# Kernel optimization log

Measured on AMD Instinct MI355X. Metric: run time of the kernel, lower is better.

Reference implementation:

```python
import math
import jax, jax.numpy as jnp
import numpy as np

B, C, H, W = 4, 64, 128, 128
A = 64           # attention_size
OUT = 64         # output_size
KS = 3           # kernel_size
M = (KS - 1) // 2
SCALE = A ** (-0.5)


def _lin(x, Wt, b):
    return x @ Wt + b


def _pos_encoding(d_model, seq_len):
    # sinusoidal PE over the k^2 neighborhood positions; d_model even here
    pos = jnp.arange(seq_len, dtype=jnp.float32)[:, None]
    div = jnp.exp(jnp.arange(0, d_model, 2, dtype=jnp.float32) * (-math.log(10000.0) / d_model))
    s = jnp.sin(pos * div)   # (seq, d/2)
    c = jnp.cos(pos * div)
    return jnp.stack([s, c], axis=-1).reshape(seq_len, d_model)  # interleaved sin/cos


def _expand_shift(k_nchw):
    # k_nchw: (b, c, h, w) -> (b, c, h, w, KS*KS) neighbor gather (zero padded)
    h, w = k_nchw.shape[2], k_nchw.shape[3]
    p = jnp.pad(k_nchw, ((0, 0), (0, 0), (M, M), (M, M)))
    slices = [p[:, :, i:i + h, j:j + w] for i in range(KS) for j in range(KS)]
    return jnp.stack(slices, axis=-1)


def setup_inputs() -> dict:
    key = jax.random.key(0)
    ks = jax.random.split(key, 12)
    sd = lambda fan_in: 1.0 / math.sqrt(fan_in)
    return {
        "x": jax.random.normal(ks[0], (B, C, H, W), jnp.float32),
        "ln_g": jnp.ones((C,), jnp.float32),
        "ln_b": jnp.zeros((C,), jnp.float32),
        "Wq": jax.random.normal(ks[1], (C, 2 * A), jnp.float32) * sd(C),
        "bq": jnp.zeros((2 * A,), jnp.float32),
        "Wq2": jax.random.normal(ks[2], (2 * A, A), jnp.float32) * sd(2 * A),
        "bq2": jnp.zeros((A,), jnp.float32),
        "Wk": jax.random.normal(ks[3], (C, 2 * A), jnp.float32) * sd(C),
        "bk": jnp.zeros((2 * A,), jnp.float32),
        "Wk2": jax.random.normal(ks[4], (2 * A, A), jnp.float32) * sd(2 * A),
        "bk2": jnp.zeros((A,), jnp.float32),
        "Wv": jax.random.normal(ks[5], (C, 2 * A), jnp.float32) * sd(C),
        "bv": jnp.zeros((2 * A,), jnp.float32),
        "Wv2": jax.random.normal(ks[6], (2 * A, OUT), jnp.float32) * sd(2 * A),
        "bv2": jnp.zeros((OUT,), jnp.float32),
        "Wpos": jax.random.normal(ks[7], (C, A), jnp.float32) * sd(C),
        "bpos": jnp.zeros((A,), jnp.float32),
        "Wposk": jax.random.normal(ks[8], (A, A), jnp.float32) * sd(A),
        "bposk": jnp.zeros((A,), jnp.float32),
    }


def reference(x, ln_g, ln_b, Wq, bq, Wq2, bq2, Wk, bk, Wk2, bk2,
              Wv, bv, Wv2, bv2, Wpos, bpos, Wposk, bposk):
    # positional embedding over the 9 neighborhood slots
    pe = _pos_encoding(C, KS * KS)                       # (9, C)
    pos_emb = jax.nn.relu(_lin(pe, Wpos, bpos))          # (9, A)

    xn = jnp.transpose(x, (0, 2, 3, 1))                  # (b, h, w, c)
    mu = jnp.mean(xn, axis=-1, keepdims=True)
    var = jnp.mean((xn - mu) ** 2, axis=-1, keepdims=True)
    xn = (xn - mu) * jax.lax.rsqrt(var + 1e-5) * ln_g + ln_b

    K = _lin(jax.nn.relu(_lin(xn, Wk, bk)), Wk2, bk2)    # (b, h, w, A)
    Ksh = _expand_shift(jnp.transpose(K, (0, 3, 1, 2)))  # (b, A, h, w, 9)
    pos_k = jnp.transpose(_lin(pos_emb, Wposk, bposk))   # (A, 9)
    Kfull = Ksh + pos_k[None, :, None, None, :]

    Q = _lin(jax.nn.relu(_lin(xn, Wq, bq)), Wq2, bq2)    # (b, h, w, A)
    V = _lin(jax.nn.relu(_lin(xn, Wv, bv)), Wv2, bv2)    # (b, h, w, OUT)
    Vsh = _expand_shift(jnp.transpose(V, (0, 3, 1, 2)))  # (b, OUT, h, w, 9)

    att = jnp.einsum('bhwa,bahwp->bphw', Q, Kfull) * SCALE
    att = jax.nn.softmax(att, axis=1)                    # softmax over 9 neighbors
    out = jnp.einsum('bchwn,bnhw->bchw', Vsh, att)       # (b, OUT, h, w)
    return out  # stride == 1 -> no subsampling
```

## Files before the change

### kernel.cpp

```cpp
#include <hip/hip_runtime.h>
#include <hip/hip_bf16.h>
#include <math.h>

typedef __attribute__((ext_vector_type(8))) short short8;
typedef __attribute__((ext_vector_type(4))) float float4v;
typedef unsigned short ushort_t;
typedef unsigned int uint_t;

#define HWPIX 16384
#define NPIX  65536

__device__ inline float b2f(ushort_t u) {
    uint_t x = ((uint_t)u) << 16;
    return __builtin_bit_cast(float, x);
}
__device__ inline ushort_t f2b(float f) {
    uint_t x = __builtin_bit_cast(uint_t, f);
    uint_t r = (x + 0x7fffu + ((x >> 16) & 1u)) >> 16;
    return (ushort_t)r;
}
__device__ inline bool probe_bf16(const void* lng) {
    return *(const uint_t*)lng == 0x3F803F80u;
}
__device__ inline float ldf(const void* p, int i, bool bf) {
    return bf ? b2f(((const ushort_t*)p)[i]) : ((const float*)p)[i];
}
__device__ inline void unpack8(uint4 u, float* f) {
    f[0] = b2f((ushort_t)(u.x & 0xffff)); f[1] = b2f((ushort_t)(u.x >> 16));
    f[2] = b2f((ushort_t)(u.y & 0xffff)); f[3] = b2f((ushort_t)(u.y >> 16));
    f[4] = b2f((ushort_t)(u.z & 0xffff)); f[5] = b2f((ushort_t)(u.z >> 16));
    f[6] = b2f((ushort_t)(u.w & 0xffff)); f[7] = b2f((ushort_t)(u.w >> 16));
}

__global__ __launch_bounds__(256) void prep_kernel(
        const void* __restrict__ Wq, const void* __restrict__ Wq2,
        const void* __restrict__ Wk, const void* __restrict__ Wk2,
        const void* __restrict__ Wv, const void* __restrict__ Wv2,
        const void* __restrict__ Wpos, const void* __restrict__ bpos,
        const void* __restrict__ Wposk, const void* __restrict__ bposk,
        const void* __restrict__ lng,
        ushort_t* __restrict__ W1f, ushort_t* __restrict__ W2f, float* __restrict__ pk) {
    bool bf = probe_bf16(lng);
    if (blockIdx.x < 96) {
        int idx = blockIdx.x * 256 + threadIdx.x;
        int chain = idx >> 13;
        int o = idx & 8191;
        const void* W1 = chain == 0 ? Wq : (chain == 1 ? Wk : Wv);
        const void* W2 = chain == 0 ? Wq2 : (chain == 1 ? Wk2 : Wv2);
        {
            int j = o & 7, L = (o >> 3) & 63, nt = (o >> 9) & 7, kc = o >> 12;
            int k = kc * 32 + ((L >> 4) << 3) + j, n = nt * 16 + (L & 15);
            W1f[chain * 8192 + o] = f2b(ldf(W1, k * 128 + n, bf));
        }
        {
            int j = o & 7, L = (o >> 3) & 63, nt = (o >> 9) & 3, kc = (o >> 11) & 3;
            int k = kc * 32 + ((L >> 4) << 3) + j, n = nt * 16 + (L & 15);
            W2f[chain * 8192 + o] = f2b(ldf(W2, k * 64 + n, bf));
        }
    } else {
        __shared__ float pe[9][64];
        __shared__ float pemb[9][64];
        int t = threadIdx.x;
        for (int it = t; it < 576; it += 256) {
            int p = it >> 6, a = it & 63;
            int i = a >> 1;
            float div = expf(-(float)(2 * i) * 0.14391156831212787f);
            float ang = (float)p * div;
            pe[p][a] = (a & 1) ? cosf(ang) : sinf(ang);
        }
        __syncthreads();
        for (int it = t; it < 576; it += 256) {
            int p = it >> 6, a = it & 63;
            float s = ldf(bpos, a, bf);
            for (int c = 0; c < 64; ++c) s += pe[p][c] * ldf(Wpos, c * 64 + a, bf);
            pemb[p][a] = fmaxf(s, 0.f);
        }
        __syncthreads();
        for (int it = t; it < 576; it += 256) {
            int p = it >> 6, a = it & 63;
            float s = ldf(bposk, a, bf);
            for (int j = 0; j < 64; ++j) s += pemb[p][j] * ldf(Wposk, j * 64 + a, bf);
            pk[a * 9 + p] = s;
        }
    }
}

__global__ __launch_bounds__(256) void lnqkv_kernel(
        const void* __restrict__ x, const void* __restrict__ g, const void* __restrict__ bb,
        const ushort_t* __restrict__ W1f, const ushort_t* __restrict__ W2f,
        const void* __restrict__ b1q, const void* __restrict__ b1k, const void* __restrict__ b1v,
        const void* __restrict__ b2q, const void* __restrict__ b2k, const void* __restrict__ b2v,
        const void* __restrict__ lng,
        ushort_t* __restrict__ Qo, ushort_t* __restrict__ Ko, ushort_t* __restrict__ Vo) {
    bool bf = probe_bf16(lng);
    int tid = threadIdx.x;
    int wave = tid >> 6, lane = tid & 63;
    int q = lane >> 4, r = lane & 15;
    int pix0 = blockIdx.x * 64 + wave * 16;
    int b = pix0 >> 14;
    int sp = (pix0 & 16383) + r;

    float xl[8], xh[8];
    if (bf) {
        const ushort_t* xb = (const ushort_t*)x + (size_t)b * 64 * HWPIX + sp;
#pragma unroll
        for (int j = 0; j < 8; ++j) {
            xl[j] = b2f(xb[(size_t)(q * 8 + j) * HWPIX]);
            xh[j] = b2f(xb[(size_t)(32 + q * 8 + j) * HWPIX]);
        }
    } else {
        const float* xb = (const float*)x + (size_t)b * 64 * HWPIX + sp;
#pragma unroll
        for (int j = 0; j < 8; ++j) {
            xl[j] = xb[(size_t)(q * 8 + j) * HWPIX];
            xh[j] = xb[(size_t)(32 + q * 8 + j) * HWPIX];
        }
    }
    float s1 = 0.f, s2 = 0.f;
#pragma unroll
    for (int j = 0; j < 8; ++j) {
        s1 += xl[j] + xh[j];
        s2 += xl[j] * xl[j] + xh[j] * xh[j];
    }
    s1 += __shfl_xor(s1, 16); s2 += __shfl_xor(s2, 16);
    s1 += __shfl_xor(s1, 32); s2 += __shfl_xor(s2, 32);
    float mu = s1 * (1.f / 64.f);
    float var = s2 * (1.f / 64.f) - mu * mu;
    float rstd = rsqrtf(var + 1e-5f);

    short8 a0, a1;
#pragma unroll
    for (int j = 0; j < 8; ++j) {
        int c = q * 8 + j;
        float v = (xl[j] - mu) * rstd * ldf(g, c, bf) + ldf(bb, c, bf);
        a0[j] = (short)f2b(v);
        c += 32;
        v = (xh[j] - mu) * rstd * ldf(g, c, bf) + ldf(bb, c, bf);
        a1[j] = (short)f2b(v);
    }

    __shared__ __align__(16) ushort_t hid[4][16][136];

#pragma unroll
    for (int chain = 0; chain < 3; ++chain) {
        const ushort_t* W1 = W1f + chain * 8192;
        const ushort_t* W2 = W2f + chain * 8192;
        const void* b1 = chain == 0 ? b1q : (chain == 1 ? b1k : b1v);
        const void* b2 = chain == 0 ? b2q : (chain == 1 ? b2k : b2v);
        ushort_t* out = chain == 0 ? Qo : (chain == 1 ? Ko : Vo);

#pragma unroll
        for (int nt = 0; nt < 8; ++nt) {
            short8 bf0 = *reinterpret_cast<const short8*>(W1 + ((0 * 8 + nt) * 64 + lane) * 8);
            short8 bf1 = *reinterpret_cast<const short8*>(W1 + ((1 * 8 + nt) * 64 + lane) * 8);
            float4v acc = {0.f, 0.f, 0.f, 0.f};
            acc = __builtin_amdgcn_mfma_f32_16x16x32_bf16(a0, bf0, acc, 0, 0, 0);
            acc = __builtin_amdgcn_mfma_f32_16x16x32_bf16(a1, bf1, acc, 0, 0, 0);
            int n = nt * 16 + r;
            float bias = ldf(b1, n, bf);
#pragma unroll
            for (int rr = 0; rr < 4; ++rr) {
                float v = fmaxf(acc[rr] + bias, 0.f);
                hid[wave][q * 4 + rr][n] = f2b(v);
            }
        }
        short8 ha[4];
#pragma unroll
        for (int kc = 0; kc < 4; ++kc)
            ha[kc] = *reinterpret_cast<const short8*>(&hid[wave][r][kc * 32 + q * 8]);

#pragma unroll
        for (int nt = 0; nt < 4; ++nt) {
            float4v acc = {0.f, 0.f, 0.f, 0.f};
#pragma unroll
            for (int kc = 0; kc < 4; ++kc) {
                short8 bfr = *reinterpret_cast<const short8*>(W2 + ((kc * 4 + nt) * 64 + lane) * 8);
                acc = __builtin_amdgcn_mfma_f32_16x16x32_bf16(ha[kc], bfr, acc, 0, 0, 0);
            }
            int n = nt * 16 + r;
            float bias = ldf(b2, n, bf);
#pragma unroll
            for (int rr = 0; rr < 4; ++rr) {
                out[(size_t)(pix0 + q * 4 + rr) * 64 + n] = f2b(acc[rr] + bias);
            }
        }
    }
}

__global__ __launch_bounds__(256) void attn_kernel(
        const ushort_t* __restrict__ Q, const ushort_t* __restrict__ K,
        const ushort_t* __restrict__ V, const float* __restrict__ pk,
        const void* __restrict__ lng, void* __restrict__ out) {
    bool bf = probe_bf16(lng);
    int p = blockIdx.x * 256 + threadIdx.x;
    int b = p >> 14;
    int sp = p & 16383;
    int h = sp >> 7, w = sp & 127;

    float v64[64];
    const ushort_t* qp = Q + (size_t)p * 64;
#pragma unroll
    for (int c0 = 0; c0 < 64; c0 += 8) {
        uint4 u = *reinterpret_cast<const uint4*>(qp + c0);
        unpack8(u, &v64[c0]);
    }

    float s[9];
#pragma unroll
    for (int n = 0; n < 9; ++n) {
        int dy = n / 3 - 1, dx = n % 3 - 1;
        int hh = h + dy, ww = w + dx;
        float dot = 0.f;
#pragma unroll
        for (int c = 0; c < 64; ++c) dot += v64[c] * pk[c * 9 + n];
        if (hh >= 0 && hh < 128 && ww >= 0 && ww < 128) {
            const ushort_t* kp = K + ((size_t)(b << 14) + (size_t)(hh * 128 + ww)) * 64;
#pragma unroll
            for (int c0 = 0; c0 < 64; c0 += 8) {
                uint4 u = *reinterpret_cast<const uint4*>(kp + c0);
                float kv[8];
                unpack8(u, kv);
#pragma unroll
                for (int j = 0; j < 8; ++j) dot += v64[c0 + j] * kv[j];
            }
        }
        s[n] = dot * 0.125f;
    }
    float m = s[0];
#pragma unroll
    for (int n = 1; n < 9; ++n) m = fmaxf(m, s[n]);
    float sum = 0.f;
#pragma unroll
    for (int n = 0; n < 9; ++n) { s[n] = expf(s[n] - m); sum += s[n]; }
    float inv = 1.f / sum;

#pragma unroll
    for (int c = 0; c < 64; ++c) v64[c] = 0.f;
#pragma unroll
    for (int n = 0; n < 9; ++n) {
        int dy = n / 3 - 1, dx = n % 3 - 1;
        int hh = h + dy, ww = w + dx;
        if (hh < 0 || hh >= 128 || ww < 0 || ww >= 128) continue;
        float a = s[n] * inv;
        const ushort_t* vp = V + ((size_t)(b << 14) + (size_t)(hh * 128 + ww)) * 64;
#pragma unroll
        for (int c0 = 0; c0 < 64; c0 += 8) {
            uint4 u = *reinterpret_cast<const uint4*>(vp + c0);
            float vv[8];
            unpack8(u, vv);
#pragma unroll
            for (int j = 0; j < 8; ++j) v64[c0 + j] += a * vv[j];
        }
    }
    if (bf) {
        ushort_t* ob = (ushort_t*)out + ((size_t)b * 64) * HWPIX + sp;
#pragma unroll
        for (int c = 0; c < 64; ++c) ob[(size_t)c * HWPIX] = f2b(v64[c]);
    } else {
        float* ob = (float*)out + ((size_t)b * 64) * HWPIX + sp;
#pragma unroll
        for (int c = 0; c < 64; ++c) ob[(size_t)c * HWPIX] = v64[c];
    }
}

extern "C" void kernel_launch(void* const* d_in, const int* in_sizes, int n_in,
                              void* d_out, int out_size, void* d_ws, size_t ws_size,
                              hipStream_t stream) {
    (void)in_sizes; (void)n_in; (void)out_size; (void)ws_size;
    const void* x     = d_in[0];
    const void* ln_g  = d_in[1];
    const void* ln_b  = d_in[2];
    const void* Wq    = d_in[3];
    const void* bq    = d_in[4];
    const void* Wq2   = d_in[5];
    const void* bq2   = d_in[6];
    const void* Wk    = d_in[7];
    const void* bk    = d_in[8];
    const void* Wk2   = d_in[9];
    const void* bk2   = d_in[10];
    const void* Wv    = d_in[11];
    const void* bv    = d_in[12];
    const void* Wv2   = d_in[13];
    const void* bv2   = d_in[14];
    const void* Wpos  = d_in[15];
    const void* bpos  = d_in[16];
    const void* Wposk = d_in[17];
    const void* bposk = d_in[18];

    char* ws = (char*)d_ws;
    ushort_t* Qo  = (ushort_t*)(ws);
    ushort_t* Ko  = (ushort_t*)(ws + (size_t)8 * 1024 * 1024);
    ushort_t* Vo  = (ushort_t*)(ws + (size_t)16 * 1024 * 1024);
    ushort_t* W1f = (ushort_t*)(ws + (size_t)24 * 1024 * 1024);
    ushort_t* W2f = (ushort_t*)(ws + (size_t)24 * 1024 * 1024 + 65536);
    float*    pk  = (float*)(ws + (size_t)24 * 1024 * 1024 + 131072);

    prep_kernel<<<97, 256, 0, stream>>>(Wq, Wq2, Wk, Wk2, Wv, Wv2,
                                        Wpos, bpos, Wposk, bposk, ln_g, W1f, W2f, pk);
    lnqkv_kernel<<<1024, 256, 0, stream>>>(x, ln_g, ln_b, W1f, W2f,
                                           bq, bk, bv, bq2, bk2, bv2, ln_g, Qo, Ko, Vo);
    attn_kernel<<<256, 256, 0, stream>>>(Qo, Ko, Vo, pk, ln_g, d_out);
}
```

Before: 174.5 us.

## Process 64 pixels per wave with register-held weight fragments and swizzled LDS

```diff
diff --git a/kernel.cpp b/kernel.cpp
--- a/kernel.cpp
+++ b/kernel.cpp
@@ -18,6 +18,9 @@
     uint_t x = __builtin_bit_cast(uint_t, f);
     uint_t r = (x + 0x7fffu + ((x >> 16) & 1u)) >> 16;
     return (ushort_t)r;
+}
+__device__ inline uint_t pack2(float a, float b) {
+    return (uint_t)f2b(a) | ((uint_t)f2b(b) << 16);
 }
 __device__ inline bool probe_bf16(const void* lng) {
     return *(const uint_t*)lng == 0x3F803F80u;
@@ -39,7 +42,7 @@
         const void* __restrict__ Wpos, const void* __restrict__ bpos,
         const void* __restrict__ Wposk, const void* __restrict__ bposk,
         const void* __restrict__ lng,
-        ushort_t* __restrict__ W1f, ushort_t* __restrict__ W2f, float* __restrict__ pk) {
+        ushort_t* __restrict__ W1A, ushort_t* __restrict__ W2A, float* __restrict__ pk) {
     bool bf = probe_bf16(lng);
     if (blockIdx.x < 96) {
         int idx = blockIdx.x * 256 + threadIdx.x;
@@ -48,14 +51,16 @@
         const void* W1 = chain == 0 ? Wq : (chain == 1 ? Wk : Wv);
         const void* W2 = chain == 0 ? Wq2 : (chain == 1 ? Wk2 : Wv2);
         {
-            int j = o & 7, L = (o >> 3) & 63, nt = (o >> 9) & 7, kc = o >> 12;
-            int k = kc * 32 + ((L >> 4) << 3) + j, n = nt * 16 + (L & 15);
-            W1f[chain * 8192 + o] = f2b(ldf(W1, k * 128 + n, bf));
+            int j = o & 7, L = (o >> 3) & 63, kc = (o >> 9) & 1, mt = (o >> 10) & 7;
+            int k = kc * 32 + ((L >> 4) << 3) + j;
+            int m = mt * 16 + (L & 15);
+            W1A[chain * 8192 + o] = f2b(ldf(W1, k * 128 + m, bf));
         }
         {
-            int j = o & 7, L = (o >> 3) & 63, nt = (o >> 9) & 3, kc = (o >> 11) & 3;
-            int k = kc * 32 + ((L >> 4) << 3) + j, n = nt * 16 + (L & 15);
-            W2f[chain * 8192 + o] = f2b(ldf(W2, k * 64 + n, bf));
+            int j = o & 7, L = (o >> 3) & 63, kc = (o >> 9) & 3, mt2 = (o >> 11) & 3;
+            int k = kc * 32 + ((L >> 4) << 3) + j;
+            int m = mt2 * 16 + (L & 15);
+            W2A[chain * 8192 + o] = f2b(ldf(W2, k * 64 + m, bf));
         }
     } else {
         __shared__ float pe[9][64];
@@ -87,7 +92,7 @@
 
 __global__ __launch_bounds__(256) void lnqkv_kernel(
         const void* __restrict__ x, const void* __restrict__ g, const void* __restrict__ bb,
-        const ushort_t* __restrict__ W1f, const ushort_t* __restrict__ W2f,
+        const ushort_t* __restrict__ W1A, const ushort_t* __restrict__ W2A,
         const void* __restrict__ b1q, const void* __restrict__ b1k, const void* __restrict__ b1v,
         const void* __restrict__ b2q, const void* __restrict__ b2k, const void* __restrict__ b2v,
         const void* __restrict__ lng,
@@ -96,92 +101,121 @@
     int tid = threadIdx.x;
     int wave = tid >> 6, lane = tid & 63;
     int q = lane >> 4, r = lane & 15;
-    int pix0 = blockIdx.x * 64 + wave * 16;
-    int b = pix0 >> 14;
-    int sp = (pix0 & 16383) + r;
-
-    float xl[8], xh[8];
-    if (bf) {
-        const ushort_t* xb = (const ushort_t*)x + (size_t)b * 64 * HWPIX + sp;
+    int base = blockIdx.x * 256 + wave * 64;
+    int b = base >> 14;
+    int spBase = base & 16383;
+
+    short8 bfr[4][2];
+#pragma unroll
+    for (int t = 0; t < 4; ++t) {
+        int sp = spBase + t * 16 + r;
+        float xl[8], xh[8];
+        if (bf) {
+            const ushort_t* xb = (const ushort_t*)x + (size_t)b * 64 * HWPIX + sp;
+#pragma unroll
+            for (int j = 0; j < 8; ++j) {
+                xl[j] = b2f(xb[(size_t)(q * 8 + j) * HWPIX]);
+                xh[j] = b2f(xb[(size_t)(32 + q * 8 + j) * HWPIX]);
+            }
+        } else {
+            const float* xb = (const float*)x + (size_t)b * 64 * HWPIX + sp;
+#pragma unroll
+            for (int j = 0; j < 8; ++j) {
+                xl[j] = xb[(size_t)(q * 8 + j) * HWPIX];
+                xh[j] = xb[(size_t)(32 + q * 8 + j) * HWPIX];
+            }
+        }
+        float s1 = 0.f, s2 = 0.f;
 #pragma unroll
         for (int j = 0; j < 8; ++j) {
-            xl[j] = b2f(xb[(size_t)(q * 8 + j) * HWPIX]);
-            xh[j] = b2f(xb[(size_t)(32 + q * 8 + j) * HWPIX]);
-        }
-    } else {
-        const float* xb = (const float*)x + (size_t)b * 64 * HWPIX + sp;
+            s1 += xl[j] + xh[j];
+            s2 += xl[j] * xl[j] + xh[j] * xh[j];
+        }
+        s1 += __shfl_xor(s1, 16); s2 += __shfl_xor(s2, 16);
+        s1 += __shfl_xor(s1, 32); s2 += __shfl_xor(s2, 32);
+        float mu = s1 * (1.f / 64.f);
+        float var = s2 * (1.f / 64.f) - mu * mu;
+        float rstd = rsqrtf(var + 1e-5f);
 #pragma unroll
         for (int j = 0; j < 8; ++j) {
-            xl[j] = xb[(size_t)(q * 8 + j) * HWPIX];
-            xh[j] = xb[(size_t)(32 + q * 8 + j) * HWPIX];
-        }
-    }
-    float s1 = 0.f, s2 = 0.f;
-#pragma unroll
-    for (int j = 0; j < 8; ++j) {
-        s1 += xl[j] + xh[j];
-        s2 += xl[j] * xl[j] + xh[j] * xh[j];
-    }
-    s1 += __shfl_xor(s1, 16); s2 += __shfl_xor(s2, 16);
-    s1 += __shfl_xor(s1, 32); s2 += __shfl_xor(s2, 32);
-    float mu = s1 * (1.f / 64.f);
-    float var = s2 * (1.f / 64.f) - mu * mu;
-    float rstd = rsqrtf(var + 1e-5f);
-
-    short8 a0, a1;
-#pragma unroll
-    for (int j = 0; j < 8; ++j) {
-        int c = q * 8 + j;
-        float v = (xl[j] - mu) * rstd * ldf(g, c, bf) + ldf(bb, c, bf);
-        a0[j] = (short)f2b(v);
-        c += 32;
-        v = (xh[j] - mu) * rstd * ldf(g, c, bf) + ldf(bb, c, bf);
-        a1[j] = (short)f2b(v);
-    }
-
-    __shared__ __align__(16) ushort_t hid[4][16][136];
-
-#pragma unroll
+            int c = q * 8 + j;
+            bfr[t][0][j] = (short)f2b((xl[j] - mu) * rstd * ldf(g, c, bf) + ldf(bb, c, bf));
+            bfr[t][1][j] = (short)f2b((xh[j] - mu) * rstd * ldf(g, c + 32, bf) + ldf(bb, c + 32, bf));
+        }
+    }
+
+    __shared__ __align__(16) ushort_t hid[4][4][16][128];
+
+#pragma unroll 1
     for (int chain = 0; chain < 3; ++chain) {
-        const ushort_t* W1 = W1f + chain * 8192;
-        const ushort_t* W2 = W2f + chain * 8192;
+        const ushort_t* W1 = W1A + chain * 8192;
+        const ushort_t* W2 = W2A + chain * 8192;
         const void* b1 = chain == 0 ? b1q : (chain == 1 ? b1k : b1v);
         const void* b2 = chain == 0 ? b2q : (chain == 1 ? b2k : b2v);
         ushort_t* out = chain == 0 ? Qo : (chain == 1 ? Ko : Vo);
 
-#pragma unroll
-        for (int nt = 0; nt < 8; ++nt) {
-            short8 bf0 = *reinterpret_cast<const short8*>(W1 + ((0 * 8 + nt) * 64 + lane) * 8);
-            short8 bf1 = *reinterpret_cast<const short8*>(W1 + ((1 * 8 + nt) * 64 + lane) * 8);
-            float4v acc = {0.f, 0.f, 0.f, 0.f};
-            acc = __builtin_amdgcn_mfma_f32_16x16x32_bf16(a0, bf0, acc, 0, 0, 0);
-            acc = __builtin_amdgcn_mfma_f32_16x16x32_bf16(a1, bf1, acc, 0, 0, 0);
-            int n = nt * 16 + r;
-            float bias = ldf(b1, n, bf);
-#pragma unroll
-            for (int rr = 0; rr < 4; ++rr) {
-                float v = fmaxf(acc[rr] + bias, 0.f);
-                hid[wave][q * 4 + rr][n] = f2b(v);
-            }
-        }
-        short8 ha[4];
-#pragma unroll
-        for (int kc = 0; kc < 4; ++kc)
-            ha[kc] = *reinterpret_cast<const short8*>(&hid[wave][r][kc * 32 + q * 8]);
-
-#pragma unroll
-        for (int nt = 0; nt < 4; ++nt) {
-            float4v acc = {0.f, 0.f, 0.f, 0.f};
-#pragma unroll
-            for (int kc = 0; kc < 4; ++kc) {
-                short8 bfr = *reinterpret_cast<const short8*>(W2 + ((kc * 4 + nt) * 64 + lane) * 8);
-                acc = __builtin_amdgcn_mfma_f32_16x16x32_bf16(ha[kc], bfr, acc, 0, 0, 0);
-            }
-            int n = nt * 16 + r;
-            float bias = ldf(b2, n, bf);
-#pragma unroll
-            for (int rr = 0; rr < 4; ++rr) {
-                out[(size_t)(pix0 + q * 4 + rr) * 64 + n] = f2b(acc[rr] + bias);
+        {
+            short8 w1[8][2];
+#pragma unroll
+            for (int mt = 0; mt < 8; ++mt)
+#pragma unroll
+                for (int kc = 0; kc < 2; ++kc)
+                    w1[mt][kc] = *reinterpret_cast<const short8*>(W1 + ((mt * 2 + kc) * 64 + lane) * 8);
+#pragma unroll
+            for (int mt = 0; mt < 8; ++mt) {
+                float bias0 = ldf(b1, mt * 16 + q * 4 + 0, bf);
+                float bias1 = ldf(b1, mt * 16 + q * 4 + 1, bf);
+                float bias2 = ldf(b1, mt * 16 + q * 4 + 2, bf);
+                float bias3 = ldf(b1, mt * 16 + q * 4 + 3, bf);
+#pragma unroll
+                for (int t = 0; t < 4; ++t) {
+                    float4v acc = {0.f, 0.f, 0.f, 0.f};
+                    acc = __builtin_amdgcn_mfma_f32_16x16x32_bf16(w1[mt][0], bfr[t][0], acc, 0, 0, 0);
+                    acc = __builtin_amdgcn_mfma_f32_16x16x32_bf16(w1[mt][1], bfr[t][1], acc, 0, 0, 0);
+                    float v0 = fmaxf(acc[0] + bias0, 0.f);
+                    float v1 = fmaxf(acc[1] + bias1, 0.f);
+                    float v2 = fmaxf(acc[2] + bias2, 0.f);
+                    float v3 = fmaxf(acc[3] + bias3, 0.f);
+                    int chunk = (2 * mt + (q >> 1)) ^ r;
+                    ushort_t* dst = &hid[wave][t][r][0] + chunk * 8 + (q & 1) * 4;
+                    uint2 d; d.x = pack2(v0, v1); d.y = pack2(v2, v3);
+                    *reinterpret_cast<uint2*>(dst) = d;
+                }
+            }
+        }
+        {
+            short8 w2[4][4];
+#pragma unroll
+            for (int mt2 = 0; mt2 < 4; ++mt2)
+#pragma unroll
+                for (int kc = 0; kc < 4; ++kc)
+                    w2[mt2][kc] = *reinterpret_cast<const short8*>(W2 + ((mt2 * 4 + kc) * 64 + lane) * 8);
+            short8 h2[4][4];
+#pragma unroll
+            for (int t = 0; t < 4; ++t)
+#pragma unroll
+                for (int kc = 0; kc < 4; ++kc) {
+                    int chunk = (4 * kc + q) ^ r;
+                    h2[t][kc] = *reinterpret_cast<const short8*>(&hid[wave][t][r][0] + chunk * 8);
+                }
+#pragma unroll
+            for (int mt2 = 0; mt2 < 4; ++mt2) {
+                float bias0 = ldf(b2, mt2 * 16 + q * 4 + 0, bf);
+                float bias1 = ldf(b2, mt2 * 16 + q * 4 + 1, bf);
+                float bias2 = ldf(b2, mt2 * 16 + q * 4 + 2, bf);
+                float bias3 = ldf(b2, mt2 * 16 + q * 4 + 3, bf);
+#pragma unroll
+                for (int t = 0; t < 4; ++t) {
+                    float4v acc = {0.f, 0.f, 0.f, 0.f};
+#pragma unroll
+                    for (int kc = 0; kc < 4; ++kc)
+                        acc = __builtin_amdgcn_mfma_f32_16x16x32_bf16(w2[mt2][kc], h2[t][kc], acc, 0, 0, 0);
+                    uint2 d;
+                    d.x = pack2(acc[0] + bias0, acc[1] + bias1);
+                    d.y = pack2(acc[2] + bias2, acc[3] + bias3);
+                    int pixel = base + t * 16 + r;
+                    *reinterpret_cast<uint2*>(out + (size_t)pixel * 64 + mt2 * 16 + q * 4) = d;
+                }
             }
         }
     }
@@ -291,13 +325,13 @@
     ushort_t* Qo  = (ushort_t*)(ws);
     ushort_t* Ko  = (ushort_t*)(ws + (size_t)8 * 1024 * 1024);
     ushort_t* Vo  = (ushort_t*)(ws + (size_t)16 * 1024 * 1024);
-    ushort_t* W1f = (ushort_t*)(ws + (size_t)24 * 1024 * 1024);
-    ushort_t* W2f = (ushort_t*)(ws + (size_t)24 * 1024 * 1024 + 65536);
+    ushort_t* W1A = (ushort_t*)(ws + (size_t)24 * 1024 * 1024);
+    ushort_t* W2A = (ushort_t*)(ws + (size_t)24 * 1024 * 1024 + 65536);
     float*    pk  = (float*)(ws + (size_t)24 * 1024 * 1024 + 131072);
 
     prep_kernel<<<97, 256, 0, stream>>>(Wq, Wq2, Wk, Wk2, Wv, Wv2,
-                                        Wpos, bpos, Wposk, bposk, ln_g, W1f, W2f, pk);
-    lnqkv_kernel<<<1024, 256, 0, stream>>>(x, ln_g, ln_b, W1f, W2f,
-                                           bq, bk, bv, bq2, bk2, bv2, ln_g, Qo, Ko, Vo);
+                                        Wpos, bpos, Wposk, bposk, ln_g, W1A, W2A, pk);
+    lnqkv_kernel<<<256, 256, 0, stream>>>(x, ln_g, ln_b, W1A, W2A,
+                                          bq, bk, bv, bq2, bk2, bv2, ln_g, Qo, Ko, Vo);
     attn_kernel<<<256, 256, 0, stream>>>(Qo, Ko, Vo, pk, ln_g, d_out);
 }
```

Result: no change. 177.9 us (+2.0%).
